# Optimization experiments

Measured on AMD Instinct MI355X. Metric: run time of the kernel, lower is better.

The kernel has to match this reference:

```python
import jax, jax.numpy as jnp
import numpy as np

KERNEL_LEN = 512
INPUT_LEN = 65536


def setup_inputs() -> dict:
    key = jax.random.key(0)
    k1, k2 = jax.random.split(key)
    x = jax.random.normal(k1, (INPUT_LEN,), dtype=jnp.float32)
    kernel = jax.random.normal(k2, (KERNEL_LEN,), dtype=jnp.float32)
    return {"input": x, "kernel": kernel}


def _dtw_row(prev, d_row):
    # prev: accumulated_cost of previous row, shape [K]
    # ac[j] = min(prev[j-1], prev[j], ac[j-1]) + d[j]
    # Let c[j] = min(prev[j-1], prev[j]) + d[j]  (prev[-1] treated as +inf,
    # which reproduces ac[i,0] = prev[0] + d[0]).
    # Then ac[j] = min(c[j], ac[j-1] + d[j])
    #            = S[j] + cummin_k<=j (c[k] - S[k]),  S = inclusive cumsum of d.
    inf = jnp.full((1,), jnp.inf, dtype=d_row.dtype)
    prev_shift = jnp.concatenate([inf, prev[:-1]])
    c = jnp.minimum(prev_shift, prev) + d_row
    S = jnp.cumsum(d_row)
    ac = S + jax.lax.cummin(c - S)
    return ac, ac[-1]


def reference(input, kernel):
    # pairwise squared distances: [input_len, kernel_len]
    d = (kernel[None, :] - input[:, None]) ** 2
    # row 0: cumulative sum along kernel axis
    prev0 = jnp.cumsum(d[0])
    # rows 1..N-1 via scan with wavefront-free min-plus row update
    _, lasts = jax.lax.scan(_dtw_row, prev0, d[1:])
    # return accumulated_cost[:, kernel_len - 1]
    return jnp.concatenate([prev0[-1:], lasts])
```

## Files before the change

kernel.cpp:

```cpp
#include <hip/hip_runtime.h>


#define K_LEN 512
#define N_LEN 65536
#define PAD_L 512
#define PAD_R 1024
#define XPAD_TOTAL (PAD_L + N_LEN + PAD_R)
#define BIGX 1e20f
#define NCHUNK 1032
#define RING 256

typedef float f32x2 __attribute__((ext_vector_type(2)));

__global__ void dtw_pad_kernel(const float* __restrict__ x, float* __restrict__ xpad) {
    int i = blockIdx.x * blockDim.x + threadIdx.x;
    if (i < XPAD_TOTAL) {
        int j = i - PAD_L;
        xpad[i] = (j >= 0 && j < N_LEN) ? x[j] : BIGX;
    }
}

__device__ __forceinline__ float dpp_wave_shr1(float oldv, float src) {
    return __int_as_float(__builtin_amdgcn_update_dpp(
        __float_as_int(oldv), __float_as_int(src), 0x138, 0xF, 0xF, false));
}
__device__ __forceinline__ float dpp_wave_shl1(float oldv, float src) {
    return __int_as_float(__builtin_amdgcn_update_dpp(
        __float_as_int(oldv), __float_as_int(src), 0x130, 0xF, 0xF, false));
}

template <bool LAST>
__device__ __forceinline__ void dtw_chunk(int c, const float* __restrict__ xl,
                                          const float* __restrict__ ldsIn,
                                          float* __restrict__ ldsOut,
                                          float k0, float k1,
                                          float& A0, float& A0p, float& A1, float& E1,
                                          float& xp, int lane, float* __restrict__ out) {
    const int t0 = c * 64;
    const int rb = (c & 3) * 64;

    float binvreg = ldsIn[(rb + lane - 1) & (RING - 1)];
    float keepreg = 0.0f;

    const f32x2* __restrict__ xl2 = (const f32x2*)(xl + t0);

    auto ITER = [&](float xf) {
        const float esh0 = dpp_wave_shr1(binvreg, E1);
        binvreg = dpp_wave_shl1(binvreg, binvreg);
        const float t0v = k0 - xf;
        const float na0 = __builtin_fmaf(t0v, t0v, fminf(A0, esh0));
        const float t1v = k1 - xp;
        const float m1  = fminf(A0p, fminf(A1, A0));
        const float na1 = __builtin_fmaf(t1v, t1v, m1);
        const float ne1 = fminf(na1, A1);
        keepreg = dpp_wave_shl1(LAST ? na1 : ne1, keepreg);
        A0p = A0; A0 = na0; A1 = na1; E1 = ne1; xp = xf;
    };

    auto LOAD8 = [&](f32x2 (&X)[8], int base) {
#pragma unroll
        for (int q = 0; q < 8; ++q) X[q] = xl2[base + q];
    };
    auto BLOCK16 = [&](const f32x2 (&X)[8]) {
#pragma unroll
        for (int q = 0; q < 8; ++q) { ITER(X[q].x); ITER(X[q].y); }
    };

    f32x2 xA[8], xB[8];
    LOAD8(xA, 0);
    LOAD8(xB, 8);
    BLOCK16(xA);
    LOAD8(xA, 16);
    BLOCK16(xB);
    LOAD8(xB, 24);
    BLOCK16(xA);
    BLOCK16(xB);

    if (!LAST) {
        ldsOut[rb + lane] = keepreg;
    } else {
        const int oi = t0 + lane - (K_LEN - 1);
        if (oi >= 0 && oi < N_LEN) out[oi] = keepreg;
    }
}

__global__ __launch_bounds__(256, 1) void dtw_main(const float* __restrict__ xpad,
                                                   const float* __restrict__ kern,
                                                   float* __restrict__ out) {
    __shared__ float lds[4 * RING];
    const float INFV = __builtin_inff();
    const int tid  = threadIdx.x;
    const int w    = __builtin_amdgcn_readfirstlane(tid) >> 6;
    const int lane = tid & 63;

    for (int i = tid; i < 4 * RING; i += 256)
        lds[i] = (i == 4 * RING - 1) ? 0.0f : INFV;
    __syncthreads();

    const int j0 = w * 128 + 2 * lane;
    const float k0 = kern[j0];
    const float k1 = kern[j0 + 1];

    const float* xl = xpad + (PAD_L - j0);
    float xp = xl[-1];

    float* ldsOut      = lds + w * RING;
    const float* ldsIn = (w == 0) ? (lds + 3 * RING) : (lds + (w - 1) * RING);

    float A0 = INFV, A0p = INFV, A1 = INFV, E1 = INFV;

    for (int S = 0; S < NCHUNK + 3; ++S) {
        const int c = S - w;
        if (c >= 0 && c < NCHUNK) {
            if (w == 3)
                dtw_chunk<true>(c, xl, ldsIn, ldsOut, k0, k1, A0, A0p, A1, E1, xp, lane, out);
            else
                dtw_chunk<false>(c, xl, ldsIn, ldsOut, k0, k1, A0, A0p, A1, E1, xp, lane, out);
        }
        if (S == 0 && tid == 0) lds[4 * RING - 1] = INFV;
        asm volatile("s_waitcnt lgkmcnt(0)\n\ts_barrier" ::: "memory");
    }
}

extern "C" void kernel_launch(void* const* d_in, const int* in_sizes, int n_in,
                              void* d_out, int out_size, void* d_ws, size_t ws_size,
                              hipStream_t stream) {
    const float* x = (const float*)d_in[0];
    const float* k = (const float*)d_in[1];
    float* xpad = (float*)d_ws;
    float* out  = (float*)d_out;
    dtw_pad_kernel<<<(XPAD_TOTAL + 255) / 256, 256, 0, stream>>>(x, xpad);
    dtw_main<<<1, 256, 0, stream>>>(xpad, k, out);
}
```

Measured before the change: 2.242 ms.

## Double-buffer chunk loads via inline asm and restructure wavefront skew loop

Replaces the in-chunk staged x loads with a register double buffer: each whole 64-element chunk is loaded by 32 inline-asm dwordx2 loads one chunk ahead, so global load latency overlaps the previous chunk's compute. The skewed wavefront schedule becomes leading and trailing barrier loops per wave, which removes the per-step c-range branch. This costs many more live VGPRs, and the last prefetch may read past the padded buffer end, though it stays inside the workspace.

```diff
diff --git a/kernel.cpp b/kernel.cpp
--- a/kernel.cpp
+++ b/kernel.cpp
@@ -29,24 +29,70 @@
         __float_as_int(oldv), __float_as_int(src), 0x130, 0xF, 0xF, false));
 }
 
+#define BARRIER() asm volatile("s_waitcnt lgkmcnt(0)\n\ts_barrier" ::: "memory")
+
+struct XBuf { f32x2 v[32]; };
+
+__device__ __forceinline__ void load_chunk(XBuf& b, const float* p) {
+    asm volatile(
+        "global_load_dwordx2 %0,  %[ad], off\n\t"
+        "global_load_dwordx2 %1,  %[ad], off offset:8\n\t"
+        "global_load_dwordx2 %2,  %[ad], off offset:16\n\t"
+        "global_load_dwordx2 %3,  %[ad], off offset:24\n\t"
+        "global_load_dwordx2 %4,  %[ad], off offset:32\n\t"
+        "global_load_dwordx2 %5,  %[ad], off offset:40\n\t"
+        "global_load_dwordx2 %6,  %[ad], off offset:48\n\t"
+        "global_load_dwordx2 %7,  %[ad], off offset:56\n\t"
+        "global_load_dwordx2 %8,  %[ad], off offset:64\n\t"
+        "global_load_dwordx2 %9,  %[ad], off offset:72\n\t"
+        "global_load_dwordx2 %10, %[ad], off offset:80\n\t"
+        "global_load_dwordx2 %11, %[ad], off offset:88\n\t"
+        "global_load_dwordx2 %12, %[ad], off offset:96\n\t"
+        "global_load_dwordx2 %13, %[ad], off offset:104\n\t"
+        "global_load_dwordx2 %14, %[ad], off offset:112\n\t"
+        "global_load_dwordx2 %15, %[ad], off offset:120\n\t"
+        "global_load_dwordx2 %16, %[ad], off offset:128\n\t"
+        "global_load_dwordx2 %17, %[ad], off offset:136\n\t"
+        "global_load_dwordx2 %18, %[ad], off offset:144\n\t"
+        "global_load_dwordx2 %19, %[ad], off offset:152\n\t"
+        "global_load_dwordx2 %20, %[ad], off offset:160\n\t"
+        "global_load_dwordx2 %21, %[ad], off offset:168\n\t"
+        "global_load_dwordx2 %22, %[ad], off offset:176\n\t"
+        "global_load_dwordx2 %23, %[ad], off offset:184\n\t"
+        "global_load_dwordx2 %24, %[ad], off offset:192\n\t"
+        "global_load_dwordx2 %25, %[ad], off offset:200\n\t"
+        "global_load_dwordx2 %26, %[ad], off offset:208\n\t"
+        "global_load_dwordx2 %27, %[ad], off offset:216\n\t"
+        "global_load_dwordx2 %28, %[ad], off offset:224\n\t"
+        "global_load_dwordx2 %29, %[ad], off offset:232\n\t"
+        "global_load_dwordx2 %30, %[ad], off offset:240\n\t"
+        "global_load_dwordx2 %31, %[ad], off offset:248"
+        : "=v"(b.v[0]),  "=v"(b.v[1]),  "=v"(b.v[2]),  "=v"(b.v[3]),
+          "=v"(b.v[4]),  "=v"(b.v[5]),  "=v"(b.v[6]),  "=v"(b.v[7]),
+          "=v"(b.v[8]),  "=v"(b.v[9]),  "=v"(b.v[10]), "=v"(b.v[11]),
+          "=v"(b.v[12]), "=v"(b.v[13]), "=v"(b.v[14]), "=v"(b.v[15]),
+          "=v"(b.v[16]), "=v"(b.v[17]), "=v"(b.v[18]), "=v"(b.v[19]),
+          "=v"(b.v[20]), "=v"(b.v[21]), "=v"(b.v[22]), "=v"(b.v[23]),
+          "=v"(b.v[24]), "=v"(b.v[25]), "=v"(b.v[26]), "=v"(b.v[27]),
+          "=v"(b.v[28]), "=v"(b.v[29]), "=v"(b.v[30]), "=v"(b.v[31])
+        : [ad] "v"(p)
+        : "memory");
+}
+
 template <bool LAST>
-__device__ __forceinline__ void dtw_chunk(int c, const float* __restrict__ xl,
-                                          const float* __restrict__ ldsIn,
-                                          float* __restrict__ ldsOut,
-                                          float k0, float k1,
-                                          float& A0, float& A0p, float& A1, float& E1,
-                                          float& xp, int lane, float* __restrict__ out) {
+__device__ __forceinline__ void compute_chunk(int c, const XBuf& b, float binv,
+                                              float k0, float k1,
+                                              float& A0, float& A0p, float& A1, float& E1,
+                                              float& xp, int lane,
+                                              float* __restrict__ ldsOut,
+                                              float* __restrict__ out) {
     const int t0 = c * 64;
     const int rb = (c & 3) * 64;
-
-    float binvreg = ldsIn[(rb + lane - 1) & (RING - 1)];
     float keepreg = 0.0f;
 
-    const f32x2* __restrict__ xl2 = (const f32x2*)(xl + t0);
-
     auto ITER = [&](float xf) {
-        const float esh0 = dpp_wave_shr1(binvreg, E1);
-        binvreg = dpp_wave_shl1(binvreg, binvreg);
+        const float esh0 = dpp_wave_shr1(binv, E1);
+        binv = dpp_wave_shl1(binv, binv);
         const float t0v = k0 - xf;
         const float na0 = __builtin_fmaf(t0v, t0v, fminf(A0, esh0));
         const float t1v = k1 - xp;
@@ -57,24 +103,8 @@
         A0p = A0; A0 = na0; A1 = na1; E1 = ne1; xp = xf;
     };
 
-    auto LOAD8 = [&](f32x2 (&X)[8], int base) {
 #pragma unroll
-        for (int q = 0; q < 8; ++q) X[q] = xl2[base + q];
-    };
-    auto BLOCK16 = [&](const f32x2 (&X)[8]) {
-#pragma unroll
-        for (int q = 0; q < 8; ++q) { ITER(X[q].x); ITER(X[q].y); }
-    };
-
-    f32x2 xA[8], xB[8];
-    LOAD8(xA, 0);
-    LOAD8(xB, 8);
-    BLOCK16(xA);
-    LOAD8(xA, 16);
-    BLOCK16(xB);
-    LOAD8(xB, 24);
-    BLOCK16(xA);
-    BLOCK16(xB);
+    for (int q = 0; q < 32; ++q) { ITER(b.v[q].x); ITER(b.v[q].y); }
 
     if (!LAST) {
         ldsOut[rb + lane] = keepreg;
@@ -109,17 +139,42 @@
 
     float A0 = INFV, A0p = INFV, A1 = INFV, E1 = INFV;
 
-    for (int S = 0; S < NCHUNK + 3; ++S) {
-        const int c = S - w;
-        if (c >= 0 && c < NCHUNK) {
+    XBuf bA, bB;
+    load_chunk(bA, xl);
+
+    for (int b = 0; b < w; ++b) BARRIER();
+
+    for (int cc = 0; cc < NCHUNK; cc += 2) {
+        {
+            asm volatile("s_waitcnt vmcnt(0)" ::: "memory");
+            __builtin_amdgcn_sched_barrier(0);
+            load_chunk(bB, xl + (cc + 1) * 64);
+            __builtin_amdgcn_sched_barrier(0);
+            const int c = cc;
+            const float binv = ldsIn[((c & 3) * 64 + lane - 1) & (RING - 1)];
             if (w == 3)
-                dtw_chunk<true>(c, xl, ldsIn, ldsOut, k0, k1, A0, A0p, A1, E1, xp, lane, out);
+                compute_chunk<true >(c, bA, binv, k0, k1, A0, A0p, A1, E1, xp, lane, ldsOut, out);
             else
-                dtw_chunk<false>(c, xl, ldsIn, ldsOut, k0, k1, A0, A0p, A1, E1, xp, lane, out);
+                compute_chunk<false>(c, bA, binv, k0, k1, A0, A0p, A1, E1, xp, lane, ldsOut, out);
+            if (cc == 0 && tid == 0) lds[4 * RING - 1] = INFV;
+            BARRIER();
         }
-        if (S == 0 && tid == 0) lds[4 * RING - 1] = INFV;
-        asm volatile("s_waitcnt lgkmcnt(0)\n\ts_barrier" ::: "memory");
+        {
+            asm volatile("s_waitcnt vmcnt(0)" ::: "memory");
+            __builtin_amdgcn_sched_barrier(0);
+            load_chunk(bA, xl + (cc + 2) * 64);
+            __builtin_amdgcn_sched_barrier(0);
+            const int c = cc + 1;
+            const float binv = ldsIn[((c & 3) * 64 + lane - 1) & (RING - 1)];
+            if (w == 3)
+                compute_chunk<true >(c, bB, binv, k0, k1, A0, A0p, A1, E1, xp, lane, ldsOut, out);
+            else
+                compute_chunk<false>(c, bB, binv, k0, k1, A0, A0p, A1, E1, xp, lane, ldsOut, out);
+            BARRIER();
+        }
     }
+
+    for (int b = 0; b < 3 - w; ++b) BARRIER();
 }
 
 extern "C" void kernel_launch(void* const* d_in, const int* in_sizes, int n_in,
```

New measurement: 2.602 ms. +16.1%, slower.

## Restructure DTW wavefront loop with cross-chunk prefetch and merged DPP ring register

Applied to the files above, without the earlier changes.

Each wave now runs its own chunk loop, with a staggered number of barriers before and after it, instead of a shared global-step loop that branches on chunk validity. Input loads become hand-written global_load_dwordx2 groups into four rotating buffers, prefetched two blocks ahead across chunk boundaries, with explicit vmcnt waits and scheduling barriers. The separate incoming-boundary and outgoing-result registers are merged into one register that is shifted once per iteration, which drops one DPP op from the serial dependency chain. This relies on inline asm and manual wait counts, so it adds register pressure and is fragile if the compiler reorders or counts outstanding loads differently.

```diff
diff --git a/kernel.cpp b/kernel.cpp
--- a/kernel.cpp
+++ b/kernel.cpp
@@ -29,58 +29,80 @@
         __float_as_int(oldv), __float_as_int(src), 0x130, 0xF, 0xF, false));
 }
 
+#define BARRIER() asm volatile("s_waitcnt lgkmcnt(0)\n\ts_barrier" ::: "memory")
+#define WAITV16() do { asm volatile("s_waitcnt vmcnt(16)" ::: "memory"); \
+                       __builtin_amdgcn_sched_barrier(0); } while (0)
+
+struct XB { f32x2 v[8]; };
+
+__device__ __forceinline__ void load_sb(XB& b, const float* p) {
+    asm volatile(
+        "global_load_dwordx2 %0, %[ad], off\n\t"
+        "global_load_dwordx2 %1, %[ad], off offset:8\n\t"
+        "global_load_dwordx2 %2, %[ad], off offset:16\n\t"
+        "global_load_dwordx2 %3, %[ad], off offset:24\n\t"
+        "global_load_dwordx2 %4, %[ad], off offset:32\n\t"
+        "global_load_dwordx2 %5, %[ad], off offset:40\n\t"
+        "global_load_dwordx2 %6, %[ad], off offset:48\n\t"
+        "global_load_dwordx2 %7, %[ad], off offset:56"
+        : "=v"(b.v[0]), "=v"(b.v[1]), "=v"(b.v[2]), "=v"(b.v[3]),
+          "=v"(b.v[4]), "=v"(b.v[5]), "=v"(b.v[6]), "=v"(b.v[7])
+        : [ad] "v"(p)
+        : "memory");
+}
+
 template <bool LAST>
-__device__ __forceinline__ void dtw_chunk(int c, const float* __restrict__ xl,
-                                          const float* __restrict__ ldsIn,
-                                          float* __restrict__ ldsOut,
-                                          float k0, float k1,
-                                          float& A0, float& A0p, float& A1, float& E1,
-                                          float& xp, int lane, float* __restrict__ out) {
-    const int t0 = c * 64;
-    const int rb = (c & 3) * 64;
+__device__ __forceinline__ void run_loop(const float* __restrict__ xl,
+                                         const float* __restrict__ ldsIn,
+                                         float* __restrict__ ldsOut,
+                                         float* __restrict__ lds,
+                                         float k0, float k1, int lane, int tid,
+                                         float* __restrict__ out) {
+    const float INFV = __builtin_inff();
+    float A0 = INFV, A0p = INFV, A1 = INFV, E1 = INFV;
+    float xp = xl[-1];
 
-    float binvreg = ldsIn[(rb + lane - 1) & (RING - 1)];
-    float keepreg = 0.0f;
-
-    const f32x2* __restrict__ xl2 = (const f32x2*)(xl + t0);
+    XB b0, b1, b2, b3;
+    float bk;
 
     auto ITER = [&](float xf) {
-        const float esh0 = dpp_wave_shr1(binvreg, E1);
-        binvreg = dpp_wave_shl1(binvreg, binvreg);
+        const float esh0 = dpp_wave_shr1(bk, E1);
         const float t0v = k0 - xf;
         const float na0 = __builtin_fmaf(t0v, t0v, fminf(A0, esh0));
         const float t1v = k1 - xp;
         const float m1  = fminf(A0p, fminf(A1, A0));
         const float na1 = __builtin_fmaf(t1v, t1v, m1);
         const float ne1 = fminf(na1, A1);
-        keepreg = dpp_wave_shl1(LAST ? na1 : ne1, keepreg);
+        bk = dpp_wave_shl1(LAST ? na1 : ne1, bk);
         A0p = A0; A0 = na0; A1 = na1; E1 = ne1; xp = xf;
     };
-
-    auto LOAD8 = [&](f32x2 (&X)[8], int base) {
+    auto COMPUTE = [&](const XB& b) {
 #pragma unroll
-        for (int q = 0; q < 8; ++q) X[q] = xl2[base + q];
-    };
-    auto BLOCK16 = [&](const f32x2 (&X)[8]) {
-#pragma unroll
-        for (int q = 0; q < 8; ++q) { ITER(X[q].x); ITER(X[q].y); }
+        for (int q = 0; q < 8; ++q) { ITER(b.v[q].x); ITER(b.v[q].y); }
     };
 
-    f32x2 xA[8], xB[8];
-    LOAD8(xA, 0);
-    LOAD8(xB, 8);
-    BLOCK16(xA);
-    LOAD8(xA, 16);
-    BLOCK16(xB);
-    LOAD8(xB, 24);
-    BLOCK16(xA);
-    BLOCK16(xB);
+    load_sb(b0, xl);
+    load_sb(b1, xl + 16);
 
-    if (!LAST) {
-        ldsOut[rb + lane] = keepreg;
-    } else {
-        const int oi = t0 + lane - (K_LEN - 1);
-        if (oi >= 0 && oi < N_LEN) out[oi] = keepreg;
+
+    for (int c = 0; c < NCHUNK; ++c) {
+        const int t0 = c * 64;
+        const int rb = (c & 3) << 6;
+        bk = ldsIn[(rb + lane - 1) & (RING - 1)];
+
+        load_sb(b2, xl + t0 + 32); WAITV16(); COMPUTE(b0);
+        load_sb(b3, xl + t0 + 48); WAITV16(); COMPUTE(b1);
+        load_sb(b0, xl + t0 + 64); WAITV16(); COMPUTE(b2);
+        load_sb(b1, xl + t0 + 80); WAITV16(); COMPUTE(b3);
+
+        if (!LAST) {
+            ldsOut[rb + lane] = bk;
+        } else {
+            const int oi = t0 + lane - (K_LEN - 1);
+            if (oi >= 0 && oi < N_LEN) out[oi] = bk;
+        }
+        if (c == 0 && tid == 0) lds[4 * RING - 1] = INFV;
+        BARRIER();
     }
 }
 
@@ -102,24 +124,18 @@
     const float k1 = kern[j0 + 1];
 
     const float* xl = xpad + (PAD_L - j0);
-    float xp = xl[-1];
 
     float* ldsOut      = lds + w * RING;
     const float* ldsIn = (w == 0) ? (lds + 3 * RING) : (lds + (w - 1) * RING);
 
-    float A0 = INFV, A0p = INFV, A1 = INFV, E1 = INFV;
+    for (int b = 0; b < w; ++b) BARRIER();
 
-    for (int S = 0; S < NCHUNK + 3; ++S) {
-        const int c = S - w;
-        if (c >= 0 && c < NCHUNK) {
-            if (w == 3)
-                dtw_chunk<true>(c, xl, ldsIn, ldsOut, k0, k1, A0, A0p, A1, E1, xp, lane, out);
-            else
-                dtw_chunk<false>(c, xl, ldsIn, ldsOut, k0, k1, A0, A0p, A1, E1, xp, lane, out);
-        }
-        if (S == 0 && tid == 0) lds[4 * RING - 1] = INFV;
-        asm volatile("s_waitcnt lgkmcnt(0)\n\ts_barrier" ::: "memory");
-    }
+    if (w == 3)
+        run_loop<true >(xl, ldsIn, ldsOut, lds, k0, k1, lane, tid, out);
+    else
+        run_loop<false>(xl, ldsIn, ldsOut, lds, k0, k1, lane, tid, out);
+
+    for (int b = 0; b < 3 - w; ++b) BARRIER();
 }
 
 extern "C" void kernel_launch(void* const* d_in, const int* in_sizes, int n_in,
```

Measured after the change: 2.328 ms. +3.8%, slower.
